# Optimization experiments

Measured on AMD Instinct MI355X. Metric: run time of the kernel, lower is better.

Reference implementation:

```python
import jax, jax.numpy as jnp
import numpy as np

# hparams (SpeechSplit-style, scaled up)
MAX_LEN_SEQ = 2048
MAX_LEN_PAD = 2560
MIN_LEN_SEG = 19
MAX_LEN_SEG = 32
MAX_NUM_SEG = MAX_LEN_SEQ // MIN_LEN_SEG + 1  # 108
B = 32
D = 80
S = MAX_LEN_SEG * 2  # 64 candidate interp positions per segment
N = B * MAX_NUM_SEG  # 3456


def setup_inputs() -> dict:
    key = jax.random.key(0)
    k1, k2, k3, k4 = jax.random.split(key, 4)
    x = jax.random.normal(k1, (B, MAX_LEN_PAD, D), dtype=jnp.float32)
    len_seq = jax.random.randint(k2, (B,), 0, MAX_LEN_SEQ, dtype=jnp.int32)
    scales_u = jax.random.uniform(k3, (N,), dtype=jnp.float32)  # uniform [0,1); +0.5 inside reference
    len_seg_raw = jax.random.randint(k4, (N, 1), 0, MAX_LEN_SEG - MIN_LEN_SEG, dtype=jnp.int32)
    return {"x": x, "len_seq": len_seq, "scales_u": scales_u, "len_seg_raw": len_seg_raw}


def reference(x, len_seq, scales_u, len_seg_raw):
    b, tx, d = x.shape
    # per-segment scaled time indices
    idx = jnp.arange(S, dtype=jnp.float32)[None, :]                     # (1, S)
    scales = scales_u + 0.5                                             # (N,) in [0.5, 1.5)
    idx_scaled = idx / scales[:, None]                                  # (N, S)
    idx_fl = jnp.floor(idx_scaled)
    lam = idx_scaled - idx_fl                                           # lerp weight (N, S)
    len_seg = len_seg_raw + MIN_LEN_SEG                                 # (N, 1) int
    idx_mask = idx_fl < (len_seg.astype(jnp.float32) - 1.0)             # within this segment
    # cumulative segment offsets per batch row
    offset = jnp.cumsum(len_seg.reshape(b, MAX_NUM_SEG), axis=-1)
    offset = jnp.pad(offset[:, :-1], ((0, 0), (1, 0))).reshape(-1, 1)   # (N, 1)
    idx_org = idx_fl + offset.astype(jnp.float32)                       # absolute source frame
    len_seq_rp = jnp.repeat(len_seq, MAX_NUM_SEG)                       # (N,)
    mask = idx_mask & (idx_org < (len_seq_rp - 1).astype(jnp.float32)[:, None])  # (N, S)

    mask_f = mask.reshape(-1)                                           # (N*S,)
    pos = jnp.cumsum(mask_f.astype(jnp.int32)) - 1                      # compacted position per element
    total = mask_f.astype(jnp.int32).sum()                              # total compacted rows

    # gather floor/ceil frames (index_1 = batch row of each flattened element)
    elem_batch = (jnp.arange(N * S, dtype=jnp.int32) // (MAX_NUM_SEG * S))
    i_fl = jnp.clip(idx_org.reshape(-1).astype(jnp.int32), 0, tx - 2)   # masked elems always in-range
    y_fl = x[elem_batch, i_fl]                                          # (N*S, D)
    y_cl = x[elem_batch, i_fl + 1]                                      # (N*S, D)
    lam_f = lam.reshape(-1, 1)
    y = (1.0 - lam_f) * y_fl + lam_f * y_cl                             # linear interp

    # boolean compaction via scatter into fixed-size buffer (masked-out rows dropped)
    write_pos = jnp.where(mask_f, pos, N * S)
    buf = jnp.zeros((N * S, d), x.dtype).at[write_pos].set(y, mode='drop')

    # reshape compacted stream to (b, total//b, d), trim/pad to MAX_LEN_PAD
    rows = total // b
    t = jnp.arange(MAX_LEN_PAD)
    gidx = jnp.arange(b)[:, None] * rows + t[None, :]                   # (b, MAX_LEN_PAD)
    valid = t[None, :] < rows
    out = jnp.where(valid[..., None], buf[jnp.clip(gidx, 0, N * S - 1)], 0.0)
    return out
```

## Files before the change

### kernel.cpp

```cpp
#include <hip/hip_runtime.h>
#include <hip/hip_bf16.h>

#define MAX_LEN_PAD 2560
#define MIN_LEN_SEG 19
#define MAX_NUM_SEG 108
#define B_ROWS      32
#define D_DIM       80
#define S_CAND      64
#define N_SEG       3456

#define WS_META      0
#define WS_SEGSTART  16
#define WS_SEGOFF    (16 + 3520)

__global__ __launch_bounds__(1024) void seg_scan_kernel(
    const int* __restrict__ len_seq, const float* __restrict__ scales_u,
    const int* __restrict__ len_seg_raw, int* __restrict__ ws)
{
    __shared__ int lenseg[N_SEG];
    __shared__ int offs[N_SEG];
    __shared__ int cnts[N_SEG];
    __shared__ int scan[1024];

    int tid = threadIdx.x;
    for (int i = tid; i < N_SEG; i += 1024) lenseg[i] = len_seg_raw[i] + MIN_LEN_SEG;
    __syncthreads();

    if (tid < B_ROWS) {
        int off = 0;
        int base = tid * MAX_NUM_SEG;
        for (int j = 0; j < MAX_NUM_SEG; ++j) {
            offs[base + j] = off;
            off += lenseg[base + j];
        }
    }
    __syncthreads();

    for (int i = tid; i < N_SEG; i += 1024) {
        float scale = scales_u[i] + 0.5f;
        int T = lenseg[i] - 1;
        int lim = len_seq[i / MAX_NUM_SEG] - 1 - offs[i];
        if (lim < T) T = lim;
        float Tf = (float)T;
        int lo = 0, hi = S_CAND;
        while (lo < hi) {
            int mid = (lo + hi) >> 1;
            float fi = floorf((float)mid / scale);
            if (fi < Tf) lo = mid + 1; else hi = mid;
        }
        cnts[i] = lo;
    }
    __syncthreads();

    int c0 = 0;
    int base4 = tid * 4;
    #pragma unroll
    for (int j = 0; j < 4; ++j) {
        int k = base4 + j;
        if (k < N_SEG) c0 += cnts[k];
    }
    scan[tid] = c0;
    __syncthreads();
    for (int off = 1; off < 1024; off <<= 1) {
        int v = scan[tid];
        if (tid >= off) v += scan[tid - off];
        __syncthreads();
        scan[tid] = v;
        __syncthreads();
    }
    int total = scan[1023];
    int excl = scan[tid] - c0;

    int* seg_start = ws + WS_SEGSTART;
    int* seg_off   = ws + WS_SEGOFF;
    int run = excl;
    #pragma unroll
    for (int j = 0; j < 4; ++j) {
        int k = base4 + j;
        if (k < N_SEG) { seg_start[k] = run; run += cnts[k]; }
    }
    if (tid == 0) {
        seg_start[N_SEG] = total;
        int rows = total / B_ROWS;
        int M = rows < MAX_LEN_PAD ? rows : MAX_LEN_PAD;
        ws[WS_META + 0] = rows;
        ws[WS_META + 1] = M;
    }
    for (int i = tid; i < N_SEG; i += 1024) seg_off[i] = offs[i];
}

__global__ __launch_bounds__(320) void fill_kernel(
    const float* __restrict__ x, const float* __restrict__ scales_u,
    const int* __restrict__ ws, float* __restrict__ out)
{
    __shared__ int   s_src[16];
    __shared__ float s_lam[16];

    const int* meta      = ws + WS_META;
    const int* seg_start = ws + WS_SEGSTART;
    const int* seg_off   = ws + WS_SEGOFF;

    int tid = threadIdx.x;
    int r_base = blockIdx.x * 16;
    int rows = meta[0];
    int M    = meta[1];

    if (tid < 16) {
        int r = r_base + tid;
        int b = r / MAX_LEN_PAD;
        int t = r - b * MAX_LEN_PAD;
        int src = -1;
        float lam = 0.0f;
        if (t < M) {
            int g = b * rows + t;
            int lo = 0, hi = N_SEG;
            while (lo < hi) {
                int mid = (lo + hi) >> 1;
                if (seg_start[mid + 1] <= g) lo = mid + 1; else hi = mid;
            }
            int n = lo;
            int s = g - seg_start[n];
            float scale = scales_u[n] + 0.5f;
            float q = (float)s / scale;
            float fi = floorf(q);
            lam = q - fi;
            int idx_org = (int)fi + seg_off[n];
            int i_fl = idx_org;
            if (i_fl < 0) i_fl = 0;
            if (i_fl > MAX_LEN_PAD - 2) i_fl = MAX_LEN_PAD - 2;
            src = (n / MAX_NUM_SEG) * MAX_LEN_PAD + i_fl;
        }
        s_src[tid] = src;
        s_lam[tid] = lam;
    }
    __syncthreads();

    int rl = tid / 20;
    int q4 = tid - rl * 20;
    int r  = r_base + rl;
    int   src = s_src[rl];
    float lam = s_lam[rl];

    float4 res;
    if (src < 0) {
        res = make_float4(0.f, 0.f, 0.f, 0.f);
    } else {
        const float4* x4 = (const float4*)x;
        float4 a = x4[src * 20 + q4];
        float4 c = x4[src * 20 + 20 + q4];
        float om = 1.0f - lam;
        res.x = om * a.x + lam * c.x;
        res.y = om * a.y + lam * c.y;
        res.z = om * a.z + lam * c.z;
        res.w = om * a.w + lam * c.w;
    }
    ((float4*)out)[r * 20 + q4] = res;
}

extern "C" void kernel_launch(void* const* d_in, const int* in_sizes, int n_in,
                              void* d_out, int out_size, void* d_ws, size_t ws_size,
                              hipStream_t stream) {
    (void)in_sizes; (void)n_in; (void)out_size; (void)ws_size;
    const float* x           = (const float*)d_in[0];
    const int*   len_seq     = (const int*)d_in[1];
    const float* scales_u    = (const float*)d_in[2];
    const int*   len_seg_raw = (const int*)d_in[3];
    float* out = (float*)d_out;
    int*   ws  = (int*)d_ws;

    seg_scan_kernel<<<1, 1024, 0, stream>>>(len_seq, scales_u, len_seg_raw, ws);

    fill_kernel<<<5120, 320, 0, stream>>>(x, scales_u, ws, out);
}
```

Baseline: 95.00 us.

## Scatter per segment instead of binary-search gather, and use wave-shuffle scans

The fill kernel now handles one segment per block and scatters each segment's interpolated rows straight to their output positions. This replaces the per-row binary search over segment starts. The same blocks also zero the padding rows past M by striding over the output. The scan kernel swaps the serial per-row offset loop and the shared-memory Hillis-Steele scan for shuffle-based wave scans with fewer barriers. In exchange, only 3456 of the 5120 blocks do interpolation work, and segments have uneven counts, so the load may be imbalanced.

New measurement: 88.31 us. 7.0% less time.

```diff
diff --git a/kernel.cpp b/kernel.cpp
--- a/kernel.cpp
+++ b/kernel.cpp
@@ -5,7 +5,6 @@
 #define MIN_LEN_SEG 19
 #define MAX_NUM_SEG 108
 #define B_ROWS      32
-#define D_DIM       80
 #define S_CAND      64
 #define N_SEG       3456
 
@@ -19,142 +18,152 @@
 {
     __shared__ int lenseg[N_SEG];
     __shared__ int offs[N_SEG];
-    __shared__ int cnts[N_SEG];
-    __shared__ int scan[1024];
+    __shared__ int wavesum[24];
 
     int tid = threadIdx.x;
     for (int i = tid; i < N_SEG; i += 1024) lenseg[i] = len_seg_raw[i] + MIN_LEN_SEG;
     __syncthreads();
 
-    if (tid < B_ROWS) {
-        int off = 0;
-        int base = tid * MAX_NUM_SEG;
-        for (int j = 0; j < MAX_NUM_SEG; ++j) {
-            offs[base + j] = off;
-            off += lenseg[base + j];
+    {
+        int row = tid >> 5, l32 = tid & 31;
+        int base = row * MAX_NUM_SEG;
+        int v[4]; int sum = 0;
+        #pragma unroll
+        for (int j = 0; j < 4; ++j) {
+            int k = l32 * 4 + j;
+            v[j] = (k < MAX_NUM_SEG) ? lenseg[base + k] : 0;
+            sum += v[j];
+        }
+        int incl = sum;
+        #pragma unroll
+        for (int d = 1; d < 32; d <<= 1) {
+            int o = __shfl_up(incl, d, 32);
+            if (l32 >= d) incl += o;
+        }
+        int run = incl - sum;
+        #pragma unroll
+        for (int j = 0; j < 4; ++j) {
+            int k = l32 * 4 + j;
+            if (k < MAX_NUM_SEG) { offs[base + k] = run; run += v[j]; }
         }
     }
     __syncthreads();
 
-    for (int i = tid; i < N_SEG; i += 1024) {
-        float scale = scales_u[i] + 0.5f;
-        int T = lenseg[i] - 1;
-        int lim = len_seq[i / MAX_NUM_SEG] - 1 - offs[i];
-        if (lim < T) T = lim;
-        float Tf = (float)T;
-        int lo = 0, hi = S_CAND;
-        while (lo < hi) {
-            int mid = (lo + hi) >> 1;
-            float fi = floorf((float)mid / scale);
-            if (fi < Tf) lo = mid + 1; else hi = mid;
+    int cnt[4] = {0, 0, 0, 0};
+    int csum = 0;
+    if (tid < N_SEG / 4) {
+        float4 sc4 = ((const float4*)scales_u)[tid];
+        float scv[4] = {sc4.x, sc4.y, sc4.z, sc4.w};
+        #pragma unroll
+        for (int j = 0; j < 4; ++j) {
+            int k = tid * 4 + j;
+            float scale = scv[j] + 0.5f;
+            int T = lenseg[k] - 1;
+            int lim = len_seq[k / MAX_NUM_SEG] - 1 - offs[k];
+            if (lim < T) T = lim;
+            float Tf = (float)T;
+            int lo = 0, hi = S_CAND;
+            while (lo < hi) {
+                int mid = (lo + hi) >> 1;
+                if (floorf((float)mid / scale) < Tf) lo = mid + 1; else hi = mid;
+            }
+            cnt[j] = lo; csum += lo;
         }
-        cnts[i] = lo;
+    }
+
+    int lane = tid & 63, wave = tid >> 6;
+    int incl = csum;
+    #pragma unroll
+    for (int d = 1; d < 64; d <<= 1) {
+        int o = __shfl_up(incl, d, 64);
+        if (lane >= d) incl += o;
+    }
+    if (lane == 63) wavesum[wave] = incl;
+    __syncthreads();
+    if (tid == 0) {
+        int run = 0;
+        #pragma unroll
+        for (int w = 0; w < 16; ++w) { int v = wavesum[w]; wavesum[w] = run; run += v; }
+        wavesum[16] = run;
     }
     __syncthreads();
-
-    int c0 = 0;
-    int base4 = tid * 4;
-    #pragma unroll
-    for (int j = 0; j < 4; ++j) {
-        int k = base4 + j;
-        if (k < N_SEG) c0 += cnts[k];
-    }
-    scan[tid] = c0;
-    __syncthreads();
-    for (int off = 1; off < 1024; off <<= 1) {
-        int v = scan[tid];
-        if (tid >= off) v += scan[tid - off];
-        __syncthreads();
-        scan[tid] = v;
-        __syncthreads();
-    }
-    int total = scan[1023];
-    int excl = scan[tid] - c0;
+    int excl = wavesum[wave] + incl - csum;
 
     int* seg_start = ws + WS_SEGSTART;
     int* seg_off   = ws + WS_SEGOFF;
-    int run = excl;
-    #pragma unroll
-    for (int j = 0; j < 4; ++j) {
-        int k = base4 + j;
-        if (k < N_SEG) { seg_start[k] = run; run += cnts[k]; }
+    if (tid < N_SEG / 4) {
+        int4 st;
+        st.x = excl;
+        st.y = st.x + cnt[0];
+        st.z = st.y + cnt[1];
+        st.w = st.z + cnt[2];
+        ((int4*)seg_start)[tid] = st;
     }
+    for (int i = tid; i < N_SEG; i += 1024) seg_off[i] = offs[i];
     if (tid == 0) {
+        int total = wavesum[16];
         seg_start[N_SEG] = total;
         int rows = total / B_ROWS;
         int M = rows < MAX_LEN_PAD ? rows : MAX_LEN_PAD;
         ws[WS_META + 0] = rows;
         ws[WS_META + 1] = M;
     }
-    for (int i = tid; i < N_SEG; i += 1024) seg_off[i] = offs[i];
 }
 
-__global__ __launch_bounds__(320) void fill_kernel(
+__global__ __launch_bounds__(320) void scatter_fill_kernel(
     const float* __restrict__ x, const float* __restrict__ scales_u,
     const int* __restrict__ ws, float* __restrict__ out)
 {
-    __shared__ int   s_src[16];
-    __shared__ float s_lam[16];
-
     const int* meta      = ws + WS_META;
     const int* seg_start = ws + WS_SEGSTART;
     const int* seg_off   = ws + WS_SEGOFF;
 
-    int tid = threadIdx.x;
-    int r_base = blockIdx.x * 16;
     int rows = meta[0];
     int M    = meta[1];
+    int tid  = threadIdx.x;
+    int rl   = tid / 20;
+    int q4   = tid - rl * 20;
+    const float4* x4   = (const float4*)x;
+    float4*       out4 = (float4*)out;
 
-    if (tid < 16) {
-        int r = r_base + tid;
-        int b = r / MAX_LEN_PAD;
-        int t = r - b * MAX_LEN_PAD;
-        int src = -1;
-        float lam = 0.0f;
-        if (t < M) {
-            int g = b * rows + t;
-            int lo = 0, hi = N_SEG;
-            while (lo < hi) {
-                int mid = (lo + hi) >> 1;
-                if (seg_start[mid + 1] <= g) lo = mid + 1; else hi = mid;
+    int n = blockIdx.x;
+    if (n < N_SEG && rows > 0) {
+        int s0  = seg_start[n];
+        int cnt = seg_start[n + 1] - s0;
+        if (cnt > 0) {
+            float scale = scales_u[n] + 0.5f;
+            int off  = seg_off[n];
+            int xrow = (n / MAX_NUM_SEG) * MAX_LEN_PAD;
+            for (int s = rl; s < cnt; s += 16) {
+                int g = s0 + s;
+                int b_out = g / rows;
+                if (b_out < B_ROWS) {
+                    int t = g - b_out * rows;
+                    if (t < MAX_LEN_PAD) {
+                        float q  = (float)s / scale;
+                        float fi = floorf(q);
+                        float lam = q - fi;
+                        int i_fl = (int)fi + off;
+                        if (i_fl > MAX_LEN_PAD - 2) i_fl = MAX_LEN_PAD - 2;
+                        int sb = (xrow + i_fl) * 20 + q4;
+                        float4 a = x4[sb];
+                        float4 c = x4[sb + 20];
+                        float om = 1.0f - lam;
+                        float4 r;
+                        r.x = om * a.x + lam * c.x;
+                        r.y = om * a.y + lam * c.y;
+                        r.z = om * a.z + lam * c.z;
+                        r.w = om * a.w + lam * c.w;
+                        out4[(b_out * MAX_LEN_PAD + t) * 20 + q4] = r;
+                    }
+                }
             }
-            int n = lo;
-            int s = g - seg_start[n];
-            float scale = scales_u[n] + 0.5f;
-            float q = (float)s / scale;
-            float fi = floorf(q);
-            lam = q - fi;
-            int idx_org = (int)fi + seg_off[n];
-            int i_fl = idx_org;
-            if (i_fl < 0) i_fl = 0;
-            if (i_fl > MAX_LEN_PAD - 2) i_fl = MAX_LEN_PAD - 2;
-            src = (n / MAX_NUM_SEG) * MAX_LEN_PAD + i_fl;
         }
-        s_src[tid] = src;
-        s_lam[tid] = lam;
     }
-    __syncthreads();
 
-    int rl = tid / 20;
-    int q4 = tid - rl * 20;
-    int r  = r_base + rl;
-    int   src = s_src[rl];
-    float lam = s_lam[rl];
-
-    float4 res;
-    if (src < 0) {
-        res = make_float4(0.f, 0.f, 0.f, 0.f);
-    } else {
-        const float4* x4 = (const float4*)x;
-        float4 a = x4[src * 20 + q4];
-        float4 c = x4[src * 20 + 20 + q4];
-        float om = 1.0f - lam;
-        res.x = om * a.x + lam * c.x;
-        res.y = om * a.y + lam * c.y;
-        res.z = om * a.z + lam * c.z;
-        res.w = om * a.w + lam * c.w;
-    }
-    ((float4*)out)[r * 20 + q4] = res;
+    int r = blockIdx.x * 16 + rl;
+    int t = (blockIdx.x % (MAX_LEN_PAD / 16)) * 16 + rl;
+    if (t >= M) out4[r * 20 + q4] = make_float4(0.f, 0.f, 0.f, 0.f);
 }
 
 extern "C" void kernel_launch(void* const* d_in, const int* in_sizes, int n_in,
@@ -170,5 +179,5 @@
 
     seg_scan_kernel<<<1, 1024, 0, stream>>>(len_seq, scales_u, len_seg_raw, ws);
 
-    fill_kernel<<<5120, 320, 0, stream>>>(x, scales_u, ws, out);
+    scatter_fill_kernel<<<5120, 320, 0, stream>>>(x, scales_u, ws, out);
 }
```

## Fuse segment scan into fill kernel, recomputing scan redundantly per block

Applied to the files above, without the earlier changes.

Merges the single-block segment scan kernel and the fill kernel into one launch. Each of the 2560 blocks of 640 threads recomputes the segment offset and count prefix sums in shared memory using wave shuffle scans, then fills 32 output rows. This removes a kernel launch, the serial single-block dependency and the workspace round trip. In exchange every block repeats about 3456 segment binary searches and the scans, which adds redundant compute and shared-memory use per block.

After: 125.3 us. 1.32x slower.

```diff
diff --git a/kernel.cpp b/kernel.cpp
--- a/kernel.cpp
+++ b/kernel.cpp
@@ -5,108 +5,124 @@
 #define MIN_LEN_SEG 19
 #define MAX_NUM_SEG 108
 #define B_ROWS      32
-#define D_DIM       80
 #define S_CAND      64
 #define N_SEG       3456
+#define SEG_PER_THR 6
+#define NTHR        640
 
-#define WS_META      0
-#define WS_SEGSTART  16
-#define WS_SEGOFF    (16 + 3520)
+__global__ __launch_bounds__(NTHR) void interp_fused_kernel(
+    const float* __restrict__ x, const int* __restrict__ len_seq,
+    const float* __restrict__ scales_u, const int* __restrict__ len_seg_raw,
+    float* __restrict__ out)
+{
+    __shared__ int   s_lg[N_SEG];
+    __shared__ float s_scale[N_SEG];
+    __shared__ int   s_start[N_SEG + 1];
+    __shared__ int   s_rowcum[B_ROWS];
+    __shared__ int   s_part[16];
+    __shared__ int   s_misc[4];
+    __shared__ int   s_src[32];
+    __shared__ float s_lam[32];
 
-__global__ __launch_bounds__(1024) void seg_scan_kernel(
-    const int* __restrict__ len_seq, const float* __restrict__ scales_u,
-    const int* __restrict__ len_seg_raw, int* __restrict__ ws)
-{
-    __shared__ int lenseg[N_SEG];
-    __shared__ int offs[N_SEG];
-    __shared__ int cnts[N_SEG];
-    __shared__ int scan[1024];
+    const int tid  = threadIdx.x;
+    const int lane = tid & 63;
+    const int wave = tid >> 6;
 
-    int tid = threadIdx.x;
-    for (int i = tid; i < N_SEG; i += 1024) lenseg[i] = len_seg_raw[i] + MIN_LEN_SEG;
-    __syncthreads();
-
-    if (tid < B_ROWS) {
-        int off = 0;
-        int base = tid * MAX_NUM_SEG;
-        for (int j = 0; j < MAX_NUM_SEG; ++j) {
-            offs[base + j] = off;
-            off += lenseg[base + j];
-        }
+    for (int i = tid; i < N_SEG; i += NTHR) {
+        s_lg[i]    = len_seg_raw[i] + MIN_LEN_SEG;
+        s_scale[i] = scales_u[i];
     }
     __syncthreads();
 
-    for (int i = tid; i < N_SEG; i += 1024) {
-        float scale = scales_u[i] + 0.5f;
-        int T = lenseg[i] - 1;
-        int lim = len_seq[i / MAX_NUM_SEG] - 1 - offs[i];
-        if (lim < T) T = lim;
-        float Tf = (float)T;
-        int lo = 0, hi = S_CAND;
-        while (lo < hi) {
-            int mid = (lo + hi) >> 1;
-            float fi = floorf((float)mid / scale);
-            if (fi < Tf) lo = mid + 1; else hi = mid;
+    int v[SEG_PER_THR];
+    int sum = 0;
+    const bool active = tid < N_SEG / SEG_PER_THR;
+    if (active) {
+        #pragma unroll
+        for (int j = 0; j < SEG_PER_THR; ++j) {
+            v[j] = s_lg[tid * SEG_PER_THR + j];
+            sum += v[j];
         }
-        cnts[i] = lo;
+    }
+    int incl = sum;
+    #pragma unroll
+    for (int d = 1; d < 64; d <<= 1) {
+        int o = __shfl_up(incl, d, 64);
+        if (lane >= d) incl += o;
+    }
+    if (lane == 63) s_part[wave] = incl;
+    __syncthreads();
+    if (tid == 0) {
+        int run = 0;
+        #pragma unroll
+        for (int w = 0; w < 10; ++w) { int p = s_part[w]; s_part[w] = run; run += p; }
+    }
+    __syncthreads();
+    int gbase = s_part[wave] + incl - sum;
+    if (active) {
+        int run = gbase;
+        #pragma unroll
+        for (int j = 0; j < SEG_PER_THR; ++j) { s_lg[tid * SEG_PER_THR + j] = run; run += v[j]; }
+    }
+    __syncthreads();
+    if (tid < B_ROWS) s_rowcum[tid] = s_lg[tid * MAX_NUM_SEG];
+    __syncthreads();
+
+    int cnt[SEG_PER_THR];
+    int csum = 0;
+    if (active) {
+        const int brow = tid / (MAX_NUM_SEG / SEG_PER_THR);
+        const int ls   = len_seq[brow];
+        int run = gbase;
+        #pragma unroll
+        for (int j = 0; j < SEG_PER_THR; ++j) {
+            int k = tid * SEG_PER_THR + j;
+            float scale = s_scale[k] + 0.5f;
+            int off = run - s_rowcum[brow];
+            run += v[j];
+            int T = v[j] - 1;
+            int lim = ls - 1 - off;
+            if (lim < T) T = lim;
+            float Tf = (float)T;
+            int lo = 0, hi = S_CAND;
+            while (lo < hi) {
+                int mid = (lo + hi) >> 1;
+                if (floorf((float)mid / scale) < Tf) lo = mid + 1; else hi = mid;
+            }
+            cnt[j] = lo; csum += lo;
+        }
+    }
+
+    int cincl = csum;
+    #pragma unroll
+    for (int d = 1; d < 64; d <<= 1) {
+        int o = __shfl_up(cincl, d, 64);
+        if (lane >= d) cincl += o;
+    }
+    if (lane == 63) s_part[wave] = cincl;
+    __syncthreads();
+    if (tid == 0) {
+        int run = 0;
+        #pragma unroll
+        for (int w = 0; w < 10; ++w) { int p = s_part[w]; s_part[w] = run; run += p; }
+        s_start[N_SEG] = run;
+        int rows = run / B_ROWS;
+        int M = rows < MAX_LEN_PAD ? rows : MAX_LEN_PAD;
+        s_misc[0] = rows;
+        s_misc[1] = M;
+    }
+    __syncthreads();
+    if (active) {
+        int run = s_part[wave] + cincl - csum;
+        #pragma unroll
+        for (int j = 0; j < SEG_PER_THR; ++j) { s_start[tid * SEG_PER_THR + j] = run; run += cnt[j]; }
     }
     __syncthreads();
 
-    int c0 = 0;
-    int base4 = tid * 4;
-    #pragma unroll
-    for (int j = 0; j < 4; ++j) {
-        int k = base4 + j;
-        if (k < N_SEG) c0 += cnts[k];
-    }
-    scan[tid] = c0;
-    __syncthreads();
-    for (int off = 1; off < 1024; off <<= 1) {
-        int v = scan[tid];
-        if (tid >= off) v += scan[tid - off];
-        __syncthreads();
-        scan[tid] = v;
-        __syncthreads();
-    }
-    int total = scan[1023];
-    int excl = scan[tid] - c0;
-
-    int* seg_start = ws + WS_SEGSTART;
-    int* seg_off   = ws + WS_SEGOFF;
-    int run = excl;
-    #pragma unroll
-    for (int j = 0; j < 4; ++j) {
-        int k = base4 + j;
-        if (k < N_SEG) { seg_start[k] = run; run += cnts[k]; }
-    }
-    if (tid == 0) {
-        seg_start[N_SEG] = total;
-        int rows = total / B_ROWS;
-        int M = rows < MAX_LEN_PAD ? rows : MAX_LEN_PAD;
-        ws[WS_META + 0] = rows;
-        ws[WS_META + 1] = M;
-    }
-    for (int i = tid; i < N_SEG; i += 1024) seg_off[i] = offs[i];
-}
-
-__global__ __launch_bounds__(320) void fill_kernel(
-    const float* __restrict__ x, const float* __restrict__ scales_u,
-    const int* __restrict__ ws, float* __restrict__ out)
-{
-    __shared__ int   s_src[16];
-    __shared__ float s_lam[16];
-
-    const int* meta      = ws + WS_META;
-    const int* seg_start = ws + WS_SEGSTART;
-    const int* seg_off   = ws + WS_SEGOFF;
-
-    int tid = threadIdx.x;
-    int r_base = blockIdx.x * 16;
-    int rows = meta[0];
-    int M    = meta[1];
-
-    if (tid < 16) {
-        int r = r_base + tid;
+    const int rows = s_misc[0];
+    const int M    = s_misc[1];
+    if (tid < 32) {
+        int r = blockIdx.x * 32 + tid;
         int b = r / MAX_LEN_PAD;
         int t = r - b * MAX_LEN_PAD;
         int src = -1;
@@ -116,30 +132,30 @@
             int lo = 0, hi = N_SEG;
             while (lo < hi) {
                 int mid = (lo + hi) >> 1;
-                if (seg_start[mid + 1] <= g) lo = mid + 1; else hi = mid;
+                if (s_start[mid + 1] <= g) lo = mid + 1; else hi = mid;
             }
             int n = lo;
-            int s = g - seg_start[n];
-            float scale = scales_u[n] + 0.5f;
-            float q = (float)s / scale;
+            int s = g - s_start[n];
+            float scale = s_scale[n] + 0.5f;
+            float q  = (float)s / scale;
             float fi = floorf(q);
             lam = q - fi;
-            int idx_org = (int)fi + seg_off[n];
-            int i_fl = idx_org;
-            if (i_fl < 0) i_fl = 0;
+            int nrow = n / MAX_NUM_SEG;
+            int off  = s_lg[n] - s_rowcum[nrow];
+            int i_fl = (int)fi + off;
             if (i_fl > MAX_LEN_PAD - 2) i_fl = MAX_LEN_PAD - 2;
-            src = (n / MAX_NUM_SEG) * MAX_LEN_PAD + i_fl;
+            src = nrow * MAX_LEN_PAD + i_fl;
         }
         s_src[tid] = src;
         s_lam[tid] = lam;
     }
     __syncthreads();
 
-    int rl = tid / 20;
-    int q4 = tid - rl * 20;
-    int r  = r_base + rl;
-    int   src = s_src[rl];
-    float lam = s_lam[rl];
+    const int rl = tid / 20;
+    const int q4 = tid - rl * 20;
+    const int r  = blockIdx.x * 32 + rl;
+    const int   src = s_src[rl];
+    const float lam = s_lam[rl];
 
     float4 res;
     if (src < 0) {
@@ -160,15 +176,12 @@
 extern "C" void kernel_launch(void* const* d_in, const int* in_sizes, int n_in,
                               void* d_out, int out_size, void* d_ws, size_t ws_size,
                               hipStream_t stream) {
-    (void)in_sizes; (void)n_in; (void)out_size; (void)ws_size;
+    (void)in_sizes; (void)n_in; (void)out_size; (void)d_ws; (void)ws_size;
     const float* x           = (const float*)d_in[0];
     const int*   len_seq     = (const int*)d_in[1];
     const float* scales_u    = (const float*)d_in[2];
     const int*   len_seg_raw = (const int*)d_in[3];
     float* out = (float*)d_out;
-    int*   ws  = (int*)d_ws;
 
-    seg_scan_kernel<<<1, 1024, 0, stream>>>(len_seq, scales_u, len_seg_raw, ws);
-
-    fill_kernel<<<5120, 320, 0, stream>>>(x, scales_u, ws, out);
+    interp_fused_kernel<<<2560, NTHR, 0, stream>>>(x, len_seq, scales_u, len_seg_raw, out);
 }
```
